# Kernel optimization log

Measured on AMD Instinct MI355X. Metric: run time of the kernel, lower is better.

The kernel has to match this reference:

```python
import jax, jax.numpy as jnp
import numpy as np

B, C, H, T, K = 8, 256, 256, 4096, 2  # batch, input_size, hidden_size, seq_len, kernel_size


def setup_inputs() -> dict:
    key = jax.random.key(0)
    ks = jax.random.split(key, 9)
    x = jax.random.normal(ks[0], (B, C, T), dtype=jnp.float32)
    w = lambda k: jax.random.normal(k, (H, C, K), dtype=jnp.float32) * 0.05
    b = lambda k: jax.random.normal(k, (H,), dtype=jnp.float32) * 0.05
    return {
        "x": x,
        "Wz": w(ks[1]), "bz": b(ks[2]),
        "Wf": w(ks[3]), "bf": b(ks[4]),
        "Wo": w(ks[5]), "bo": b(ks[6]),
        "Wi": w(ks[7]), "bi": b(ks[8]),
    }


def _causal_conv(x, W, b):
    # x: [B, C, T], W: [H, C, K]; left-pad by K-1 zeros == torch.cat([zeros, x]) then valid conv
    k = W.shape[-1]
    y = jax.lax.conv_general_dilated(
        x, W, window_strides=(1,), padding=[(k - 1, 0)],
        dimension_numbers=("NCH", "OIH", "NCH"))
    return y + b[None, :, None]


def reference(x, Wz, bz, Wf, bf, Wo, bo, Wi, bi):
    z = jnp.tanh(_causal_conv(x, Wz, bz))          # [B, H, T]
    f = jax.nn.sigmoid(_causal_conv(x, Wf, bf))    # zoneout=0 -> plain sigmoid
    o = jax.nn.sigmoid(_causal_conv(x, Wo, bo))
    i = jax.nn.sigmoid(_causal_conv(x, Wi, bi))    # computed as in original; unused for 'fo' pooling
    del i

    # fo-pooling recurrence: c_t = f_t * c_{t-1} + (1 - f_t) * z_t ; h_t = o_t * c_t
    f_tbh = jnp.transpose(f, (2, 0, 1))  # [T, B, H]
    z_tbh = jnp.transpose(z, (2, 0, 1))
    c0 = jnp.zeros((x.shape[0], Wz.shape[0]), dtype=x.dtype)

    def step(c_prev, fz):
        f_t, z_t = fz
        c_t = f_t * c_prev + (1.0 - f_t) * z_t
        return c_t, c_t

    _, cs = jax.lax.scan(step, c0, (f_tbh, z_tbh))  # [T, B, H]
    c = jnp.transpose(cs, (1, 2, 0))                # [B, H, T]
    h = o * c
    return (h, c)
```

## Files before the change

kernel.cpp:

```cpp
#include <hip/hip_runtime.h>


typedef unsigned short ushort_t;
typedef __attribute__((ext_vector_type(8))) short short8_t;
typedef __attribute__((ext_vector_type(4))) float f32x4;

#define B_ 8
#define C_ 256
#define H_ 256
#define T_ 4096
#define TCH 32
#define NCH 128

__device__ __forceinline__ unsigned short f2bf(float f) {
  unsigned int u = __float_as_uint(f);
  u += 0x7fffu + ((u >> 16) & 1u);
  return (unsigned short)(u >> 16);
}
__device__ __forceinline__ float sigm(float v) { return 1.f / (1.f + __expf(-v)); }
__device__ __forceinline__ float tanh_f(float v) { return 2.f / (1.f + __expf(-2.f * v)) - 1.f; }

__device__ __forceinline__ void gl16(const ushort_t* g, ushort_t* l) {
  __builtin_amdgcn_global_load_lds(
      (const __attribute__((address_space(1))) unsigned int*)g,
      (__attribute__((address_space(3))) unsigned int*)l, 16, 0, 0);
}

__global__ __launch_bounds__(256) void qrnn_p1(const float* __restrict__ x,
                                               ushort_t* __restrict__ xp) {
  __shared__ float tile[32][129];
  const int tid = threadIdx.x;
  const int b = blockIdx.z, c0 = blockIdx.y * 32, t0 = blockIdx.x * 128;
#pragma unroll
  for (int p = 0; p < 4; ++p) {
    const int j = tid + p * 256;
    const int c = j >> 5, q = j & 31;
    float4 v = *reinterpret_cast<const float4*>(x + ((size_t)(b * C_ + c0 + c)) * T_ + t0 + q * 4);
    tile[c][q * 4 + 0] = v.x; tile[c][q * 4 + 1] = v.y;
    tile[c][q * 4 + 2] = v.z; tile[c][q * 4 + 3] = v.w;
  }
  __syncthreads();
  const int t = tid >> 1, ch = (tid & 1) * 16;
  ushort_t o[16];
#pragma unroll
  for (int i = 0; i < 16; ++i) o[i] = f2bf(tile[ch + i][t]);
  ushort_t* dst = xp + ((size_t)b * (T_ + 1) + 1 + t0 + t) * C_ + c0 + ch;
  *reinterpret_cast<uint4*>(dst) = *reinterpret_cast<uint4*>(&o[0]);
  *reinterpret_cast<uint4*>(dst + 8) = *reinterpret_cast<uint4*>(&o[8]);
}

__global__ __launch_bounds__(256) void qrnn_p2(const float* __restrict__ Wz,
                                               const float* __restrict__ Wf,
                                               const float* __restrict__ Wo,
                                               ushort_t* __restrict__ wc,
                                               ushort_t* __restrict__ xp) {
  const int idx = blockIdx.x * 256 + threadIdx.x;
  if (blockIdx.x == 0) {
#pragma unroll
    for (int b = 0; b < B_; ++b) xp[((size_t)b * (T_ + 1)) * C_ + threadIdx.x] = 0;
  }
  const int g = idx >> 17;
  const int rem = idx & 131071;
  const int h = rem >> 9;
  const int kp = rem & 511;
  const int c = kp & 255;
  const int tap = (kp < 256) ? 1 : 0;
  const float* W = (g == 0) ? Wz : ((g == 1) ? Wf : Wo);
  wc[idx] = f2bf(W[((size_t)h * C_ + c) * 2 + tap]);
}

__global__ __launch_bounds__(256) void qrnn_gates(const ushort_t* __restrict__ xp,
                                                  const ushort_t* __restrict__ wc,
                                                  const float* __restrict__ bz,
                                                  const float* __restrict__ bfv,
                                                  const float* __restrict__ bo,
                                                  float* __restrict__ zfo) {
  __shared__ ushort_t As[2][128 * 32];
  __shared__ ushort_t Bs[2][128 * 32];
  const int tid = threadIdx.x;
  const int lane = tid & 63;
  const int wid = tid >> 6;
  const int wm = wid >> 1, wn = wid & 1;
  const int l15 = lane & 15, g4 = lane >> 4;
  const int b = blockIdx.z;
  const int m0 = blockIdx.y * 128;
  const int t0 = blockIdx.x * 128;

  const int j0 = wid * 128 + lane;
  const int j1 = j0 + 64;
  const int r0 = j0 >> 2, s0 = (j0 & 3) ^ ((r0 >> 1) & 3);
  const int r1 = j1 >> 2, s1 = (j1 & 3) ^ ((r1 >> 1) & 3);
  const ushort_t* asrc0 = wc + (size_t)(m0 + r0) * 512 + s0 * 8;
  const ushort_t* asrc1 = wc + (size_t)(m0 + r1) * 512 + s1 * 8;
  const ushort_t* bsrc0 = xp + ((size_t)b * (T_ + 1) + t0 + r0) * C_ + s0 * 8;
  const ushort_t* bsrc1 = xp + ((size_t)b * (T_ + 1) + t0 + r1) * C_ + s1 * 8;
  const int dA0 = (wid * 128) * 8;
  const int dA1 = (wid * 128 + 64) * 8;

  f32x4 acc[4][4];
#pragma unroll
  for (int i = 0; i < 4; ++i)
#pragma unroll
    for (int j = 0; j < 4; ++j) acc[i][j] = (f32x4){0.f, 0.f, 0.f, 0.f};

  const int swz = (l15 >> 1) & 3;
  const int aslot = (g4 ^ swz) * 8;

  {
    gl16(asrc0, &As[0][dA0]);
    gl16(asrc1, &As[0][dA1]);
    gl16(bsrc0 + C_, &Bs[0][dA0]);
    gl16(bsrc1 + C_, &Bs[0][dA1]);
  }
  __syncthreads();

#pragma unroll
  for (int ks = 0; ks < 16; ++ks) {
    const int cur = ks & 1;
    if (ks < 15) {
      const int nk = ks + 1;
      const int ak = nk * 32;
      const int bk = (nk >= 8) ? (ak - 256) : (C_ + ak);
      gl16(asrc0 + ak, &As[cur ^ 1][dA0]);
      gl16(asrc1 + ak, &As[cur ^ 1][dA1]);
      gl16(bsrc0 + bk, &Bs[cur ^ 1][dA0]);
      gl16(bsrc1 + bk, &Bs[cur ^ 1][dA1]);
    }
    short8_t a[4], bb[4];
#pragma unroll
    for (int mi = 0; mi < 4; ++mi) {
      const int row = wm * 64 + mi * 16 + l15;
      a[mi] = *reinterpret_cast<const short8_t*>(&As[cur][row * 32 + aslot]);
    }
#pragma unroll
    for (int ni = 0; ni < 4; ++ni) {
      const int row = wn * 64 + ni * 16 + l15;
      bb[ni] = *reinterpret_cast<const short8_t*>(&Bs[cur][row * 32 + aslot]);
    }
#pragma unroll
    for (int mi = 0; mi < 4; ++mi)
#pragma unroll
      for (int ni = 0; ni < 4; ++ni)
        acc[mi][ni] = __builtin_amdgcn_mfma_f32_16x16x32_bf16(a[mi], bb[ni], acc[mi][ni], 0, 0, 0);
    __syncthreads();
  }

  const int gate = m0 >> 8;
  const float* bias = (gate == 0) ? bz : ((gate == 1) ? bfv : bo);
  const int hb = (m0 & 255) + wm * 64;
  float* obase = zfo + ((size_t)(gate * B_ + b)) * H_ * T_;
#pragma unroll
  for (int mi = 0; mi < 4; ++mi) {
#pragma unroll
    for (int r4 = 0; r4 < 4; ++r4) {
      const int h = hb + mi * 16 + g4 * 4 + r4;
      const float bvv = bias[h];
      float* rowp = obase + (size_t)h * T_ + t0 + wn * 64 + l15;
#pragma unroll
      for (int ni = 0; ni < 4; ++ni) {
        float v = acc[mi][ni][r4] + bvv;
        v = (gate == 0) ? tanh_f(v) : sigm(v);
        rowp[ni * 16] = v;
      }
    }
  }
}

__global__ __launch_bounds__(256) void qrnn_s1(const float* __restrict__ zfo,
                                               float* __restrict__ aggP,
                                               float* __restrict__ aggC) {
  __shared__ float lf[256][33];
  __shared__ float lz[256][33];
  const int tid = threadIdx.x;
  const int chunk = blockIdx.x;
  const int b = blockIdx.y;
  const int t0 = chunk * TCH;
  const float* zbase = zfo + (size_t)b * H_ * T_;
  const float* fbase = zfo + (size_t)(B_ + b) * H_ * T_;
  const int lr = tid >> 3, lc = (tid & 7) * 4;
#pragma unroll
  for (int pass = 0; pass < 8; ++pass) {
    const int row = pass * 32 + lr;
    float4 fv = *reinterpret_cast<const float4*>(fbase + (size_t)row * T_ + t0 + lc);
    float4 zv = *reinterpret_cast<const float4*>(zbase + (size_t)row * T_ + t0 + lc);
    lf[row][lc] = fv.x; lf[row][lc + 1] = fv.y; lf[row][lc + 2] = fv.z; lf[row][lc + 3] = fv.w;
    lz[row][lc] = zv.x; lz[row][lc + 1] = zv.y; lz[row][lc + 2] = zv.z; lz[row][lc + 3] = zv.w;
  }
  __syncthreads();
  float c = 0.f, p = 1.f;
#pragma unroll
  for (int t = 0; t < TCH; ++t) {
    const float f = lf[tid][t], z = lz[tid][t];
    c = f * (c - z) + z;
    p *= f;
  }
  aggP[((size_t)b * NCH + chunk) * H_ + tid] = p;
  aggC[((size_t)b * NCH + chunk) * H_ + tid] = c;
}

__global__ __launch_bounds__(256) void qrnn_s2(const float* __restrict__ aggP,
                                               const float* __restrict__ aggC,
                                               float* __restrict__ cin) {
  const int b = blockIdx.x, h = threadIdx.x;
  float carry = 0.f;
  for (int jb = 0; jb < NCH; jb += 8) {
    float P[8], Cv[8];
#pragma unroll
    for (int u = 0; u < 8; ++u) {
      P[u] = aggP[((size_t)b * NCH + jb + u) * H_ + h];
      Cv[u] = aggC[((size_t)b * NCH + jb + u) * H_ + h];
    }
#pragma unroll
    for (int u = 0; u < 8; ++u) {
      cin[((size_t)b * NCH + jb + u) * H_ + h] = carry;
      carry = Cv[u] + P[u] * carry;
    }
  }
}

__global__ __launch_bounds__(256) void qrnn_s3(const float* __restrict__ zfo,
                                               const float* __restrict__ cin,
                                               float* __restrict__ outc,
                                               float* __restrict__ outh) {
  __shared__ float lz[128][33];
  __shared__ float lf[128][33];
  __shared__ float lo[128][33];
  const int tid = threadIdx.x;
  const int chunk = blockIdx.x;
  const int h0 = blockIdx.y * 128;
  const int b = blockIdx.z;
  const int t0 = chunk * TCH;
  const float* zb = zfo + (size_t)b * H_ * T_;
  const float* fb = zfo + (size_t)(B_ + b) * H_ * T_;
  const float* ob = zfo + (size_t)(2 * B_ + b) * H_ * T_;
#pragma unroll
  for (int i = 0; i < 4; ++i) {
    const int j = tid + i * 256;
    const int row = j >> 3, c4 = (j & 7) * 4;
    const size_t goff = (size_t)(h0 + row) * T_ + t0 + c4;
    float4 zv = *reinterpret_cast<const float4*>(zb + goff);
    float4 fv = *reinterpret_cast<const float4*>(fb + goff);
    float4 ov = *reinterpret_cast<const float4*>(ob + goff);
    lz[row][c4] = zv.x; lz[row][c4 + 1] = zv.y; lz[row][c4 + 2] = zv.z; lz[row][c4 + 3] = zv.w;
    lf[row][c4] = fv.x; lf[row][c4 + 1] = fv.y; lf[row][c4 + 2] = fv.z; lf[row][c4 + 3] = fv.w;
    lo[row][c4] = ov.x; lo[row][c4 + 1] = ov.y; lo[row][c4 + 2] = ov.z; lo[row][c4 + 3] = ov.w;
  }
  __syncthreads();
  if (tid < 128) {
    float c = cin[((size_t)b * NCH + chunk) * H_ + h0 + tid];
#pragma unroll
    for (int t = 0; t < TCH; ++t) {
      const float f = lf[tid][t], z = lz[tid][t];
      c = f * (c - z) + z;
      lz[tid][t] = c;
      lf[tid][t] = lo[tid][t] * c;
    }
  }
  __syncthreads();
  float* cb = outc + (size_t)b * H_ * T_;
  float* hb = outh + (size_t)b * H_ * T_;
#pragma unroll
  for (int i = 0; i < 4; ++i) {
    const int j = tid + i * 256;
    const int row = j >> 3, c4 = (j & 7) * 4;
    const size_t goff = (size_t)(h0 + row) * T_ + t0 + c4;
    float4 cv = make_float4(lz[row][c4], lz[row][c4 + 1], lz[row][c4 + 2], lz[row][c4 + 3]);
    float4 hv = make_float4(lf[row][c4], lf[row][c4 + 1], lf[row][c4 + 2], lf[row][c4 + 3]);
    *reinterpret_cast<float4*>(cb + goff) = cv;
    *reinterpret_cast<float4*>(hb + goff) = hv;
  }
}

extern "C" void kernel_launch(void* const* d_in, const int* in_sizes, int n_in,
                              void* d_out, int out_size, void* d_ws, size_t ws_size,
                              hipStream_t stream) {
  const float* x  = (const float*)d_in[0];
  const float* Wz = (const float*)d_in[1];
  const float* bz = (const float*)d_in[2];
  const float* Wf = (const float*)d_in[3];
  const float* bfv= (const float*)d_in[4];
  const float* Wo = (const float*)d_in[5];
  const float* bo = (const float*)d_in[6];

  float* outh = (float*)d_out;
  float* outc = outh + (size_t)B_ * H_ * T_;

  constexpr size_t XP_OFF  = 0;
  constexpr size_t WC_OFF  = 16781312;
  constexpr size_t ZFO_OFF = 17567744;
  constexpr size_t AGP_OFF = 118231040;
  constexpr size_t AGC_OFF = 119279616;
  constexpr size_t CIN_OFF = 120328192;
  constexpr size_t WS_NEED = 121376768;
  if (ws_size < WS_NEED) return;

  ushort_t* xp  = (ushort_t*)((char*)d_ws + XP_OFF);
  ushort_t* wcp = (ushort_t*)((char*)d_ws + WC_OFF);
  float* zfo  = (float*)((char*)d_ws + ZFO_OFF);
  float* aggP = (float*)((char*)d_ws + AGP_OFF);
  float* aggC = (float*)((char*)d_ws + AGC_OFF);
  float* cin  = (float*)((char*)d_ws + CIN_OFF);

  qrnn_p1<<<dim3(T_ / 128, C_ / 32, B_), 256, 0, stream>>>(x, xp);
  qrnn_p2<<<dim3((3 * H_ * 512) / 256), 256, 0, stream>>>(Wz, Wf, Wo, wcp, xp);
  qrnn_gates<<<dim3(T_ / 128, 6, B_), 256, 0, stream>>>(xp, wcp, bz, bfv, bo, zfo);
  qrnn_s1<<<dim3(NCH, B_), 256, 0, stream>>>(zfo, aggP, aggC);
  qrnn_s2<<<dim3(B_), 256, 0, stream>>>(aggP, aggC, cin);
  qrnn_s3<<<dim3(NCH, 2, B_), 256, 0, stream>>>(zfo, cin, outc, outh);
}
```

Baseline: 109.0 us.

## Deepen GEMM K-loop prefetch to two stages with explicit waitcnt barriers

Restructures the conv-as-GEMM main loop so global-to-LDS loads for step ks+2 are issued into the buffer just consumed, right after fragments are read into registers. Explicit vmcnt/lgkmcnt waits and raw s_barrier calls replace __syncthreads, and s_setprio raises wave priority around the MFMA block. The aim is to keep more memory traffic in flight and overlap it with matrix math. The cost is fragile hand-tuned wait counts and an extra barrier per iteration.

```diff
diff --git a/kernel.cpp b/kernel.cpp
--- a/kernel.cpp
+++ b/kernel.cpp
@@ -106,26 +106,22 @@
   const int swz = (l15 >> 1) & 3;
   const int aslot = (g4 ^ swz) * 8;
 
-  {
-    gl16(asrc0, &As[0][dA0]);
-    gl16(asrc1, &As[0][dA1]);
-    gl16(bsrc0 + C_, &Bs[0][dA0]);
-    gl16(bsrc1 + C_, &Bs[0][dA1]);
-  }
-  __syncthreads();
+  gl16(asrc0, &As[0][dA0]);
+  gl16(asrc1, &As[0][dA1]);
+  gl16(bsrc0 + C_, &Bs[0][dA0]);
+  gl16(bsrc1 + C_, &Bs[0][dA1]);
+  gl16(asrc0 + 32, &As[1][dA0]);
+  gl16(asrc1 + 32, &As[1][dA1]);
+  gl16(bsrc0 + C_ + 32, &Bs[1][dA0]);
+  gl16(bsrc1 + C_ + 32, &Bs[1][dA1]);
+  asm volatile("s_waitcnt vmcnt(4)" ::: "memory");
+  __builtin_amdgcn_sched_barrier(0);
+  __builtin_amdgcn_s_barrier();
+  __builtin_amdgcn_sched_barrier(0);
 
 #pragma unroll
   for (int ks = 0; ks < 16; ++ks) {
     const int cur = ks & 1;
-    if (ks < 15) {
-      const int nk = ks + 1;
-      const int ak = nk * 32;
-      const int bk = (nk >= 8) ? (ak - 256) : (C_ + ak);
-      gl16(asrc0 + ak, &As[cur ^ 1][dA0]);
-      gl16(asrc1 + ak, &As[cur ^ 1][dA1]);
-      gl16(bsrc0 + bk, &Bs[cur ^ 1][dA0]);
-      gl16(bsrc1 + bk, &Bs[cur ^ 1][dA1]);
-    }
     short8_t a[4], bb[4];
 #pragma unroll
     for (int mi = 0; mi < 4; ++mi) {
@@ -137,12 +133,33 @@
       const int row = wn * 64 + ni * 16 + l15;
       bb[ni] = *reinterpret_cast<const short8_t*>(&Bs[cur][row * 32 + aslot]);
     }
+    asm volatile("s_waitcnt lgkmcnt(0)" ::: "memory");
+    __builtin_amdgcn_sched_barrier(0);
+    __builtin_amdgcn_s_barrier();
+    __builtin_amdgcn_sched_barrier(0);
+    if (ks < 14) {
+      const int nk = ks + 2;
+      const int ak = nk * 32;
+      const int bk = (nk >= 8) ? (ak - 256) : (C_ + ak);
+      gl16(asrc0 + ak, &As[cur][dA0]);
+      gl16(asrc1 + ak, &As[cur][dA1]);
+      gl16(bsrc0 + bk, &Bs[cur][dA0]);
+      gl16(bsrc1 + bk, &Bs[cur][dA1]);
+    }
+    __builtin_amdgcn_s_setprio(1);
 #pragma unroll
     for (int mi = 0; mi < 4; ++mi)
 #pragma unroll
       for (int ni = 0; ni < 4; ++ni)
         acc[mi][ni] = __builtin_amdgcn_mfma_f32_16x16x32_bf16(a[mi], bb[ni], acc[mi][ni], 0, 0, 0);
-    __syncthreads();
+    __builtin_amdgcn_s_setprio(0);
+    if (ks < 14)
+      asm volatile("s_waitcnt vmcnt(4)" ::: "memory");
+    else
+      asm volatile("s_waitcnt vmcnt(0)" ::: "memory");
+    __builtin_amdgcn_sched_barrier(0);
+    __builtin_amdgcn_s_barrier();
+    __builtin_amdgcn_sched_barrier(0);
   }
 
   const int gate = m0 >> 8;
```

After: 106.6 us. 1.02x faster.

## Prepack GEMM operands in MFMA fragment layout and store z/o gates as bf16

Applied to the files above, without the earlier changes.

Packs x (both conv taps) and weights straight into per-lane MFMA fragment order, so the gate GEMM loads operands directly from global memory with no LDS staging or barriers. One 512-thread block now covers all 768 gate rows for a 64-step time tile. The z and o gate intermediates are stored as bf16 while f stays fp32, cutting intermediate traffic for the scan kernels. In exchange the packed x buffer holds both taps, so it is twice as large, and z/o lose precision, which may affect accuracy.

```diff
diff --git a/kernel.cpp b/kernel.cpp
--- a/kernel.cpp
+++ b/kernel.cpp
@@ -17,180 +17,164 @@
   u += 0x7fffu + ((u >> 16) & 1u);
   return (unsigned short)(u >> 16);
 }
+__device__ __forceinline__ float bf2f(unsigned short u) {
+  return __uint_as_float(((unsigned int)u) << 16);
+}
 __device__ __forceinline__ float sigm(float v) { return 1.f / (1.f + __expf(-v)); }
 __device__ __forceinline__ float tanh_f(float v) { return 2.f / (1.f + __expf(-2.f * v)) - 1.f; }
 
-__device__ __forceinline__ void gl16(const ushort_t* g, ushort_t* l) {
-  __builtin_amdgcn_global_load_lds(
-      (const __attribute__((address_space(1))) unsigned int*)g,
-      (__attribute__((address_space(3))) unsigned int*)l, 16, 0, 0);
-}
-
-__global__ __launch_bounds__(256) void qrnn_p1(const float* __restrict__ x,
-                                               ushort_t* __restrict__ xp) {
-  __shared__ float tile[32][129];
+__global__ __launch_bounds__(256) void qrnn_pack_x(const float* __restrict__ x,
+                                                   ushort_t* __restrict__ xq) {
+  __shared__ float tile[32][132];
   const int tid = threadIdx.x;
-  const int b = blockIdx.z, c0 = blockIdx.y * 32, t0 = blockIdx.x * 128;
-#pragma unroll
-  for (int p = 0; p < 4; ++p) {
-    const int j = tid + p * 256;
-    const int c = j >> 5, q = j & 31;
-    float4 v = *reinterpret_cast<const float4*>(x + ((size_t)(b * C_ + c0 + c)) * T_ + t0 + q * 4);
-    tile[c][q * 4 + 0] = v.x; tile[c][q * 4 + 1] = v.y;
-    tile[c][q * 4 + 2] = v.z; tile[c][q * 4 + 3] = v.w;
+  const int t0 = blockIdx.x * 128, c0 = blockIdx.y * 32, b = blockIdx.z;
+#pragma unroll
+  for (int p = 0; p < 5; ++p) {
+    const int idx = tid + p * 256;
+    if (idx < 1056) {
+      const int row = idx / 33, q = idx % 33;
+      const int tg = t0 - 4 + q * 4;
+      float4 v = make_float4(0.f, 0.f, 0.f, 0.f);
+      if (tg >= 0)
+        v = *reinterpret_cast<const float4*>(x + ((size_t)(b * C_ + c0 + row)) * T_ + tg);
+      tile[row][q * 4 + 0] = v.x; tile[row][q * 4 + 1] = v.y;
+      tile[row][q * 4 + 2] = v.z; tile[row][q * 4 + 3] = v.w;
+    }
   }
   __syncthreads();
-  const int t = tid >> 1, ch = (tid & 1) * 16;
-  ushort_t o[16];
-#pragma unroll
-  for (int i = 0; i < 16; ++i) o[i] = f2bf(tile[ch + i][t]);
-  ushort_t* dst = xp + ((size_t)b * (T_ + 1) + 1 + t0 + t) * C_ + c0 + ch;
-  *reinterpret_cast<uint4*>(dst) = *reinterpret_cast<uint4*>(&o[0]);
-  *reinterpret_cast<uint4*>(dst + 8) = *reinterpret_cast<uint4*>(&o[8]);
-}
-
-__global__ __launch_bounds__(256) void qrnn_p2(const float* __restrict__ Wz,
-                                               const float* __restrict__ Wf,
-                                               const float* __restrict__ Wo,
-                                               ushort_t* __restrict__ wc,
-                                               ushort_t* __restrict__ xp) {
+  const int ks0 = c0 >> 5;
+#pragma unroll
+  for (int q2 = 0; q2 < 2; ++q2) {
+    const int p = tid + q2 * 256;
+    const int tfl = p >> 6, lane = p & 63;
+    const int l15 = lane & 15, g8 = (lane >> 4) * 8;
+    const int tcol = tfl * 16 + l15;
+    ushort_t o0[8], o1[8];
+#pragma unroll
+    for (int j = 0; j < 8; ++j) {
+      o0[j] = f2bf(tile[g8 + j][tcol + 4]);
+      o1[j] = f2bf(tile[g8 + j][tcol + 3]);
+    }
+    const int tf = (t0 >> 4) + tfl;
+    ushort_t* d0 = xq + ((size_t)((b * 256 + tf) * 16 + ks0) * 64 + lane) * 8;
+    ushort_t* d1 = xq + ((size_t)((b * 256 + tf) * 16 + 8 + ks0) * 64 + lane) * 8;
+    *reinterpret_cast<uint4*>(d0) = *reinterpret_cast<uint4*>(&o0[0]);
+    *reinterpret_cast<uint4*>(d1) = *reinterpret_cast<uint4*>(&o1[0]);
+  }
+}
+
+__global__ __launch_bounds__(256) void qrnn_pack_w(const float* __restrict__ Wz,
+                                                   const float* __restrict__ Wf,
+                                                   const float* __restrict__ Wo,
+                                                   ushort_t* __restrict__ aq) {
   const int idx = blockIdx.x * 256 + threadIdx.x;
-  if (blockIdx.x == 0) {
-#pragma unroll
-    for (int b = 0; b < B_; ++b) xp[((size_t)b * (T_ + 1)) * C_ + threadIdx.x] = 0;
-  }
-  const int g = idx >> 17;
-  const int rem = idx & 131071;
-  const int h = rem >> 9;
-  const int kp = rem & 511;
-  const int c = kp & 255;
-  const int tap = (kp < 256) ? 1 : 0;
+  const int lane = idx & 63;
+  const int ks = (idx >> 6) & 15;
+  const int mf = idx >> 10;
+  const int g = mf >> 4;
+  const int h = (mf & 15) * 16 + (lane & 15);
   const float* W = (g == 0) ? Wz : ((g == 1) ? Wf : Wo);
-  wc[idx] = f2bf(W[((size_t)h * C_ + c) * 2 + tap]);
-}
-
-__global__ __launch_bounds__(256) void qrnn_gates(const ushort_t* __restrict__ xp,
-                                                  const ushort_t* __restrict__ wc,
-                                                  const float* __restrict__ bz,
-                                                  const float* __restrict__ bfv,
-                                                  const float* __restrict__ bo,
-                                                  float* __restrict__ zfo) {
-  __shared__ ushort_t As[2][128 * 32];
-  __shared__ ushort_t Bs[2][128 * 32];
+  ushort_t o[8];
+#pragma unroll
+  for (int j = 0; j < 8; ++j) {
+    const int k = ks * 32 + (lane >> 4) * 8 + j;
+    const int c = k & 255;
+    const int tap = (k < 256) ? 1 : 0;
+    o[j] = f2bf(W[((size_t)h * C_ + c) * 2 + tap]);
+  }
+  *reinterpret_cast<uint4*>(aq + (size_t)idx * 8) = *reinterpret_cast<uint4*>(&o[0]);
+}
+
+__global__ __launch_bounds__(512, 2) void qrnn_g(const ushort_t* __restrict__ aq,
+                                                 const ushort_t* __restrict__ xq,
+                                                 const float* __restrict__ bz,
+                                                 const float* __restrict__ bfv,
+                                                 const float* __restrict__ bo,
+                                                 float* __restrict__ fb,
+                                                 ushort_t* __restrict__ zb,
+                                                 ushort_t* __restrict__ ob) {
   const int tid = threadIdx.x;
   const int lane = tid & 63;
-  const int wid = tid >> 6;
-  const int wm = wid >> 1, wn = wid & 1;
+  const int w = tid >> 6;
   const int l15 = lane & 15, g4 = lane >> 4;
-  const int b = blockIdx.z;
-  const int m0 = blockIdx.y * 128;
-  const int t0 = blockIdx.x * 128;
-
-  const int j0 = wid * 128 + lane;
-  const int j1 = j0 + 64;
-  const int r0 = j0 >> 2, s0 = (j0 & 3) ^ ((r0 >> 1) & 3);
-  const int r1 = j1 >> 2, s1 = (j1 & 3) ^ ((r1 >> 1) & 3);
-  const ushort_t* asrc0 = wc + (size_t)(m0 + r0) * 512 + s0 * 8;
-  const ushort_t* asrc1 = wc + (size_t)(m0 + r1) * 512 + s1 * 8;
-  const ushort_t* bsrc0 = xp + ((size_t)b * (T_ + 1) + t0 + r0) * C_ + s0 * 8;
-  const ushort_t* bsrc1 = xp + ((size_t)b * (T_ + 1) + t0 + r1) * C_ + s1 * 8;
-  const int dA0 = (wid * 128) * 8;
-  const int dA1 = (wid * 128 + 64) * 8;
-
-  f32x4 acc[4][4];
-#pragma unroll
-  for (int i = 0; i < 4; ++i)
-#pragma unroll
-    for (int j = 0; j < 4; ++j) acc[i][j] = (f32x4){0.f, 0.f, 0.f, 0.f};
-
-  const int swz = (l15 >> 1) & 3;
-  const int aslot = (g4 ^ swz) * 8;
-
-  {
-    gl16(asrc0, &As[0][dA0]);
-    gl16(asrc1, &As[0][dA1]);
-    gl16(bsrc0 + C_, &Bs[0][dA0]);
-    gl16(bsrc1 + C_, &Bs[0][dA1]);
-  }
-  __syncthreads();
-
-#pragma unroll
+  const int tt = blockIdx.x, b = blockIdx.y;
+
+  const short8_t* Abase = reinterpret_cast<const short8_t*>(aq) + (size_t)(6 * w) * 16 * 64 + lane;
+  const short8_t* Bbase =
+      reinterpret_cast<const short8_t*>(xq) + (size_t)((b * 256 + tt * 4) * 16) * 64 + lane;
+
+  f32x4 acc[6][4];
+#pragma unroll
+  for (int i = 0; i < 6; ++i)
+#pragma unroll
+    for (int n = 0; n < 4; ++n) acc[i][n] = (f32x4){0.f, 0.f, 0.f, 0.f};
+
+#pragma unroll 2
   for (int ks = 0; ks < 16; ++ks) {
-    const int cur = ks & 1;
-    if (ks < 15) {
-      const int nk = ks + 1;
-      const int ak = nk * 32;
-      const int bk = (nk >= 8) ? (ak - 256) : (C_ + ak);
-      gl16(asrc0 + ak, &As[cur ^ 1][dA0]);
-      gl16(asrc1 + ak, &As[cur ^ 1][dA1]);
-      gl16(bsrc0 + bk, &Bs[cur ^ 1][dA0]);
-      gl16(bsrc1 + bk, &Bs[cur ^ 1][dA1]);
-    }
-    short8_t a[4], bb[4];
-#pragma unroll
-    for (int mi = 0; mi < 4; ++mi) {
-      const int row = wm * 64 + mi * 16 + l15;
-      a[mi] = *reinterpret_cast<const short8_t*>(&As[cur][row * 32 + aslot]);
-    }
-#pragma unroll
-    for (int ni = 0; ni < 4; ++ni) {
-      const int row = wn * 64 + ni * 16 + l15;
-      bb[ni] = *reinterpret_cast<const short8_t*>(&Bs[cur][row * 32 + aslot]);
-    }
-#pragma unroll
-    for (int mi = 0; mi < 4; ++mi)
-#pragma unroll
-      for (int ni = 0; ni < 4; ++ni)
-        acc[mi][ni] = __builtin_amdgcn_mfma_f32_16x16x32_bf16(a[mi], bb[ni], acc[mi][ni], 0, 0, 0);
-    __syncthreads();
-  }
-
-  const int gate = m0 >> 8;
-  const float* bias = (gate == 0) ? bz : ((gate == 1) ? bfv : bo);
-  const int hb = (m0 & 255) + wm * 64;
-  float* obase = zfo + ((size_t)(gate * B_ + b)) * H_ * T_;
-#pragma unroll
-  for (int mi = 0; mi < 4; ++mi) {
-#pragma unroll
-    for (int r4 = 0; r4 < 4; ++r4) {
-      const int h = hb + mi * 16 + g4 * 4 + r4;
-      const float bvv = bias[h];
-      float* rowp = obase + (size_t)h * T_ + t0 + wn * 64 + l15;
-#pragma unroll
-      for (int ni = 0; ni < 4; ++ni) {
-        float v = acc[mi][ni][r4] + bvv;
-        v = (gate == 0) ? tanh_f(v) : sigm(v);
-        rowp[ni * 16] = v;
+    short8_t a[6], bb[4];
+#pragma unroll
+    for (int i = 0; i < 6; ++i) a[i] = Abase[(size_t)(i * 16 + ks) * 64];
+#pragma unroll
+    for (int n = 0; n < 4; ++n) bb[n] = Bbase[(size_t)(n * 16 + ks) * 64];
+#pragma unroll
+    for (int i = 0; i < 6; ++i)
+#pragma unroll
+      for (int n = 0; n < 4; ++n)
+        acc[i][n] = __builtin_amdgcn_mfma_f32_16x16x32_bf16(a[i], bb[n], acc[i][n], 0, 0, 0);
+  }
+
+#pragma unroll
+  for (int i = 0; i < 6; ++i) {
+    const int mf = 6 * w + i;
+    const int g = mf >> 4;
+    const int hb0 = (mf & 15) * 16;
+    const float* bias = (g == 0) ? bz : ((g == 1) ? bfv : bo);
+    float bv[4];
+#pragma unroll
+    for (int r = 0; r < 4; ++r) bv[r] = bias[hb0 + g4 * 4 + r];
+#pragma unroll
+    for (int n = 0; n < 4; ++n) {
+      const int t = tt * 64 + n * 16 + l15;
+#pragma unroll
+      for (int r = 0; r < 4; ++r) {
+        const int h = hb0 + g4 * 4 + r;
+        const float v = acc[i][n][r] + bv[r];
+        const size_t off = ((size_t)b * H_ + h) * T_ + t;
+        if (g == 0)      zb[off] = f2bf(tanh_f(v));
+        else if (g == 1) fb[off] = sigm(v);
+        else             ob[off] = f2bf(sigm(v));
       }
     }
   }
 }
 
-__global__ __launch_bounds__(256) void qrnn_s1(const float* __restrict__ zfo,
+__global__ __launch_bounds__(256) void qrnn_s1(const float* __restrict__ fb,
+                                               const ushort_t* __restrict__ zb,
                                                float* __restrict__ aggP,
                                                float* __restrict__ aggC) {
   __shared__ float lf[256][33];
-  __shared__ float lz[256][33];
+  __shared__ ushort_t lzs[256][36];
   const int tid = threadIdx.x;
   const int chunk = blockIdx.x;
   const int b = blockIdx.y;
   const int t0 = chunk * TCH;
-  const float* zbase = zfo + (size_t)b * H_ * T_;
-  const float* fbase = zfo + (size_t)(B_ + b) * H_ * T_;
+  const float* fbase = fb + (size_t)b * H_ * T_;
+  const ushort_t* zbase = zb + (size_t)b * H_ * T_;
   const int lr = tid >> 3, lc = (tid & 7) * 4;
 #pragma unroll
   for (int pass = 0; pass < 8; ++pass) {
     const int row = pass * 32 + lr;
     float4 fv = *reinterpret_cast<const float4*>(fbase + (size_t)row * T_ + t0 + lc);
-    float4 zv = *reinterpret_cast<const float4*>(zbase + (size_t)row * T_ + t0 + lc);
+    uint2 zv = *reinterpret_cast<const uint2*>(zbase + (size_t)row * T_ + t0 + lc);
     lf[row][lc] = fv.x; lf[row][lc + 1] = fv.y; lf[row][lc + 2] = fv.z; lf[row][lc + 3] = fv.w;
-    lz[row][lc] = zv.x; lz[row][lc + 1] = zv.y; lz[row][lc + 2] = zv.z; lz[row][lc + 3] = zv.w;
+    lzs[row][lc] = (ushort_t)(zv.x & 0xffff); lzs[row][lc + 1] = (ushort_t)(zv.x >> 16);
+    lzs[row][lc + 2] = (ushort_t)(zv.y & 0xffff); lzs[row][lc + 3] = (ushort_t)(zv.y >> 16);
   }
   __syncthreads();
   float c = 0.f, p = 1.f;
 #pragma unroll
   for (int t = 0; t < TCH; ++t) {
-    const float f = lf[tid][t], z = lz[tid][t];
+    const float f = lf[tid][t], z = bf2f(lzs[tid][t]);
     c = f * (c - z) + z;
     p *= f;
   }
@@ -218,42 +202,46 @@
   }
 }
 
-__global__ __launch_bounds__(256) void qrnn_s3(const float* __restrict__ zfo,
+__global__ __launch_bounds__(256) void qrnn_s3(const float* __restrict__ fb,
+                                               const ushort_t* __restrict__ zb,
+                                               const ushort_t* __restrict__ ob,
                                                const float* __restrict__ cin,
                                                float* __restrict__ outc,
                                                float* __restrict__ outh) {
-  __shared__ float lz[128][33];
   __shared__ float lf[128][33];
-  __shared__ float lo[128][33];
+  __shared__ ushort_t lzs[128][36];
+  __shared__ ushort_t los[128][36];
   const int tid = threadIdx.x;
   const int chunk = blockIdx.x;
   const int h0 = blockIdx.y * 128;
   const int b = blockIdx.z;
   const int t0 = chunk * TCH;
-  const float* zb = zfo + (size_t)b * H_ * T_;
-  const float* fb = zfo + (size_t)(B_ + b) * H_ * T_;
-  const float* ob = zfo + (size_t)(2 * B_ + b) * H_ * T_;
+  const float* fbase = fb + (size_t)b * H_ * T_;
+  const ushort_t* zbase = zb + (size_t)b * H_ * T_;
+  const ushort_t* obase = ob + (size_t)b * H_ * T_;
 #pragma unroll
   for (int i = 0; i < 4; ++i) {
     const int j = tid + i * 256;
     const int row = j >> 3, c4 = (j & 7) * 4;
     const size_t goff = (size_t)(h0 + row) * T_ + t0 + c4;
-    float4 zv = *reinterpret_cast<const float4*>(zb + goff);
-    float4 fv = *reinterpret_cast<const float4*>(fb + goff);
-    float4 ov = *reinterpret_cast<const float4*>(ob + goff);
-    lz[row][c4] = zv.x; lz[row][c4 + 1] = zv.y; lz[row][c4 + 2] = zv.z; lz[row][c4 + 3] = zv.w;
+    float4 fv = *reinterpret_cast<const float4*>(fbase + goff);
+    uint2 zv = *reinterpret_cast<const uint2*>(zbase + goff);
+    uint2 ov = *reinterpret_cast<const uint2*>(obase + goff);
     lf[row][c4] = fv.x; lf[row][c4 + 1] = fv.y; lf[row][c4 + 2] = fv.z; lf[row][c4 + 3] = fv.w;
-    lo[row][c4] = ov.x; lo[row][c4 + 1] = ov.y; lo[row][c4 + 2] = ov.z; lo[row][c4 + 3] = ov.w;
+    lzs[row][c4] = (ushort_t)(zv.x & 0xffff); lzs[row][c4 + 1] = (ushort_t)(zv.x >> 16);
+    lzs[row][c4 + 2] = (ushort_t)(zv.y & 0xffff); lzs[row][c4 + 3] = (ushort_t)(zv.y >> 16);
+    los[row][c4] = (ushort_t)(ov.x & 0xffff); los[row][c4 + 1] = (ushort_t)(ov.x >> 16);
+    los[row][c4 + 2] = (ushort_t)(ov.y & 0xffff); los[row][c4 + 3] = (ushort_t)(ov.y >> 16);
   }
   __syncthreads();
   if (tid < 128) {
     float c = cin[((size_t)b * NCH + chunk) * H_ + h0 + tid];
 #pragma unroll
     for (int t = 0; t < TCH; ++t) {
-      const float f = lf[tid][t], z = lz[tid][t];
+      const float f = lf[tid][t], z = bf2f(lzs[tid][t]);
       c = f * (c - z) + z;
-      lz[tid][t] = c;
-      lf[tid][t] = lo[tid][t] * c;
+      lf[tid][t] = c;
+      lzs[tid][t] = f2bf(bf2f(los[tid][t]) * c);
     }
   }
   __syncthreads();
@@ -264,8 +252,9 @@
     const int j = tid + i * 256;
     const int row = j >> 3, c4 = (j & 7) * 4;
     const size_t goff = (size_t)(h0 + row) * T_ + t0 + c4;
-    float4 cv = make_float4(lz[row][c4], lz[row][c4 + 1], lz[row][c4 + 2], lz[row][c4 + 3]);
-    float4 hv = make_float4(lf[row][c4], lf[row][c4 + 1], lf[row][c4 + 2], lf[row][c4 + 3]);
+    float4 cv = make_float4(lf[row][c4], lf[row][c4 + 1], lf[row][c4 + 2], lf[row][c4 + 3]);
+    float4 hv = make_float4(bf2f(los[row][c4]) * cv.x, bf2f(los[row][c4 + 1]) * cv.y,
+                            bf2f(los[row][c4 + 2]) * cv.z, bf2f(los[row][c4 + 3]) * cv.w);
     *reinterpret_cast<float4*>(cb + goff) = cv;
     *reinterpret_cast<float4*>(hb + goff) = hv;
   }
@@ -285,26 +274,30 @@
   float* outh = (float*)d_out;
   float* outc = outh + (size_t)B_ * H_ * T_;
 
-  constexpr size_t XP_OFF  = 0;
-  constexpr size_t WC_OFF  = 16781312;
-  constexpr size_t ZFO_OFF = 17567744;
-  constexpr size_t AGP_OFF = 118231040;
-  constexpr size_t AGC_OFF = 119279616;
-  constexpr size_t CIN_OFF = 120328192;
-  constexpr size_t WS_NEED = 121376768;
+  constexpr size_t XQ_OFF  = 0;
+  constexpr size_t AQ_OFF  = 33554432;
+  constexpr size_t FB_OFF  = 34340864;
+  constexpr size_t ZB_OFF  = 67895296;
+  constexpr size_t OB_OFF  = 84672512;
+  constexpr size_t AGP_OFF = 101449728;
+  constexpr size_t AGC_OFF = 102498304;
+  constexpr size_t CIN_OFF = 103546880;
+  constexpr size_t WS_NEED = 104595456;
   if (ws_size < WS_NEED) return;
 
-  ushort_t* xp  = (ushort_t*)((char*)d_ws + XP_OFF);
-  ushort_t* wcp = (ushort_t*)((char*)d_ws + WC_OFF);
-  float* zfo  = (float*)((char*)d_ws + ZFO_OFF);
-  float* aggP = (float*)((char*)d_ws + AGP_OFF);
-  float* aggC = (float*)((char*)d_ws + AGC_OFF);
-  float* cin  = (float*)((char*)d_ws + CIN_OFF);
-
-  qrnn_p1<<<dim3(T_ / 128, C_ / 32, B_), 256, 0, stream>>>(x, xp);
-  qrnn_p2<<<dim3((3 * H_ * 512) / 256), 256, 0, stream>>>(Wz, Wf, Wo, wcp, xp);
-  qrnn_gates<<<dim3(T_ / 128, 6, B_), 256, 0, stream>>>(xp, wcp, bz, bfv, bo, zfo);
-  qrnn_s1<<<dim3(NCH, B_), 256, 0, stream>>>(zfo, aggP, aggC);
+  ushort_t* xq = (ushort_t*)((char*)d_ws + XQ_OFF);
+  ushort_t* aq = (ushort_t*)((char*)d_ws + AQ_OFF);
+  float* fbuf  = (float*)((char*)d_ws + FB_OFF);
+  ushort_t* zb = (ushort_t*)((char*)d_ws + ZB_OFF);
+  ushort_t* ob = (ushort_t*)((char*)d_ws + OB_OFF);
+  float* aggP  = (float*)((char*)d_ws + AGP_OFF);
+  float* aggC  = (float*)((char*)d_ws + AGC_OFF);
+  float* cin   = (float*)((char*)d_ws + CIN_OFF);
+
+  qrnn_pack_x<<<dim3(T_ / 128, C_ / 32, B_), 256, 0, stream>>>(x, xq);
+  qrnn_pack_w<<<dim3(192), 256, 0, stream>>>(Wz, Wf, Wo, aq);
+  qrnn_g<<<dim3(T_ / 64, B_), 512, 0, stream>>>(aq, xq, bz, bfv, bo, fbuf, zb, ob);
+  qrnn_s1<<<dim3(NCH, B_), 256, 0, stream>>>(fbuf, zb, aggP, aggC);
   qrnn_s2<<<dim3(B_), 256, 0, stream>>>(aggP, aggC, cin);
-  qrnn_s3<<<dim3(NCH, 2, B_), 256, 0, stream>>>(zfo, cin, outc, outh);
-}
+  qrnn_s3<<<dim3(NCH, 2, B_), 256, 0, stream>>>(fbuf, zb, ob, cin, outc, outh);
+}
```

Result: slower. 125.3 us (+15.0%).
